# Performance work log

Hardware: AMD Instinct MI355X
Metric: run time of the kernel (lower is better)

Reference implementation:

```python
import jax, jax.numpy as jnp
import numpy as np

GROUP_SIZE = 16
OUT_FEATURES = 8192
IN_FEATURES = 8192


def block_dequantize_min_bit(x_quant_packed, normalization):
    """Unpack 3-bit values (8 values per 3 bytes) and dequantize per-group.

    x_quant_packed: [n_groups, group_size*3//8] int (byte values 0..255)
    normalization:  [n_groups, 1] float
    returns flat float32 vector of length n_groups*group_size.
    """
    normalization = normalization.astype(jnp.float32)
    packed_width = x_quant_packed.shape[1]
    group_size = packed_width * 8 // 3
    b = x_quant_packed.astype(jnp.int32).reshape(-1, 3)
    b0, b1, b2 = b[:, 0], b[:, 1], b[:, 2]
    v0 = (b0 >> 5) & 7
    v1 = (b0 >> 2) & 7
    v2 = ((b0 & 3) << 1) | ((b1 >> 7) & 1)
    v3 = (b1 >> 4) & 7
    v4 = (b1 >> 1) & 7
    v5 = ((b1 & 1) << 2) | ((b2 >> 6) & 3)
    v6 = (b2 >> 3) & 7
    v7 = b2 & 7
    unpacked = jnp.stack([v0, v1, v2, v3, v4, v5, v6, v7], axis=1)  # [-1, 8]
    x_quant = unpacked.reshape(-1, group_size).astype(jnp.float32)
    x_norm = x_quant / 7.0
    x = x_norm * 2.0 * normalization - normalization
    return x.reshape(-1)


def setup_inputs() -> dict:
    key = jax.random.key(0)
    k1, k2, k3, k4 = jax.random.split(key, 4)
    n_groups = OUT_FEATURES * IN_FEATURES // GROUP_SIZE
    x = jax.random.normal(k1, (64, IN_FEATURES), dtype=jnp.float32)
    weight_q3 = jax.random.randint(k2, (n_groups, GROUP_SIZE * 3 // 8), 0, 256, dtype=jnp.int32)
    # positive per-group max-abs scales (quantizer stores abs().max())
    weight_norm = jax.random.uniform(k3, (n_groups, 1), dtype=jnp.float32, minval=0.01, maxval=1.0)
    bias = jax.random.normal(k4, (OUT_FEATURES,), dtype=jnp.float32)
    return {"x": x, "weight_q3": weight_q3, "weight_norm": weight_norm, "bias": bias}


def reference(x, weight_q3, weight_norm, bias):
    w = block_dequantize_min_bit(weight_q3, weight_norm).reshape(OUT_FEATURES, IN_FEATURES)
    # F.linear: y = x @ W^T + b
    return jnp.einsum('bi,oi->bo', x, w) + bias
```

## Files before the change

kernel.cpp:

```cpp
#include <hip/hip_runtime.h>
#include <hip/hip_bf16.h>


#define BATCH   64
#define IN_F    8192
#define OUT_F   8192

#define PK_BYTES 6144
#define PA_BYTES 8192
#define BUF_BYTES (PK_BYTES + PA_BYTES)

typedef __attribute__((ext_vector_type(8))) short bf16x8;
typedef __attribute__((ext_vector_type(4))) float f32x4;

__device__ __forceinline__ ushort f2bf(float f) {
  union { float f; unsigned u; } a; a.f = f;
  unsigned r = a.u + 0x7fffu + ((a.u >> 16) & 1u);
  return (ushort)(r >> 16);
}

__device__ __forceinline__ void gl_lds16(const void* g, void* l) {
  __builtin_amdgcn_global_load_lds((const __attribute__((address_space(1))) void*)g,
                                   (__attribute__((address_space(3))) void*)l, 16, 0, 0);
}

__global__ void __launch_bounds__(256) xcvt_kernel(const float* __restrict__ x,
                                                   ushort* __restrict__ xb) {
  int i = blockIdx.x * 256 + threadIdx.x;
  float4 v = ((const float4*)x)[i];
  ushort4 o;
  o.x = f2bf(v.x); o.y = f2bf(v.y); o.z = f2bf(v.z); o.w = f2bf(v.w);
  ((ushort4*)xb)[i] = o;
}

__device__ __forceinline__ bf16x8 dqfrag(int b0, int b1, int b2, float nrm) {
  float c1 = nrm * (2.0f / 7.0f);
  float c0 = nrm;
  int v0 = (b0 >> 5) & 7;
  int v1 = (b0 >> 2) & 7;
  int v2 = ((b0 & 3) << 1) | ((b1 >> 7) & 1);
  int v3 = (b1 >> 4) & 7;
  int v4 = (b1 >> 1) & 7;
  int v5 = ((b1 & 1) << 2) | ((b2 >> 6) & 3);
  int v6 = (b2 >> 3) & 7;
  int v7 = b2 & 7;
  union { __hip_bfloat162 h[4]; bf16x8 v; } r;
  r.h[0] = __float22bfloat162_rn(make_float2(fmaf((float)v0, c1, -c0), fmaf((float)v1, c1, -c0)));
  r.h[1] = __float22bfloat162_rn(make_float2(fmaf((float)v2, c1, -c0), fmaf((float)v3, c1, -c0)));
  r.h[2] = __float22bfloat162_rn(make_float2(fmaf((float)v4, c1, -c0), fmaf((float)v5, c1, -c0)));
  r.h[3] = __float22bfloat162_rn(make_float2(fmaf((float)v6, c1, -c0), fmaf((float)v7, c1, -c0)));
  return r.v;
}

template <int KS>
__global__ void __launch_bounds__(256) gemm3b_kernel(const ushort* __restrict__ xb,
                                                     const int* __restrict__ wq,
                                                     const float* __restrict__ wnorm,
                                                     float* __restrict__ partial) {
  constexpr int K_SLICE = IN_F / KS;
  constexpr int NTILE   = K_SLICE / 64;
  constexpr int NGROW   = K_SLICE / 16;

  __shared__ __align__(16) char  LDS[2][BUF_BYTES];
  __shared__ __align__(16) float NRM[64 * NGROW];

  const int tid  = threadIdx.x;
  const int lane = tid & 63;
  const int w    = tid >> 6;
  const int l15  = lane & 15;
  const int h    = lane >> 4;
  const int nb64 = blockIdx.x * 64;
  const int s    = blockIdx.y;
  const int kbase = s * K_SLICE;
  const int kg0   = kbase >> 4;

  const char*  wqp = (const char*)wq + (size_t)nb64 * 12288 + (size_t)kg0 * 24;
  const float* wnp = wnorm + (size_t)nb64 * 512 + kg0;
  const char*  xbp = (const char*)xb + (size_t)kbase * 2;

  f32x4 acc[4];
  #pragma unroll
  for (int m = 0; m < 4; ++m) acc[m] = (f32x4){0.f, 0.f, 0.f, 0.f};

  {
    constexpr int ROWB = NGROW * 4;
    constexpr int NDM  = (64 * ROWB) / 4096;
    #pragma unroll
    for (int i = 0; i < NDM; ++i) {
      int t   = tid * 16 + i * 4096;
      int row = t / ROWB;
      int off = t % ROWB;
      float4 v = *(const float4*)((const char*)wnp + (size_t)row * 2048 + off);
      *(float4*)((char*)NRM + t) = v;
    }
  }

#define STAGE_PK_CHUNK(BUF, KT, C)                                            \
  do {                                                                        \
    int t   = (C) * 1024 + lane * 16;                                         \
    int row = (int)(((unsigned)t * 43691u) >> 22);                            \
    int off = t - row * 96;                                                   \
    gl_lds16(wqp + (size_t)row * 12288 + (KT) * 96 + off,                     \
             &LDS[BUF][(C) * 1024]);                                          \
  } while (0)

#define STAGE(BUF, KT)                                                        \
  do {                                                                        \
    STAGE_PK_CHUNK(BUF, KT, w);                                               \
    if (w < 2) STAGE_PK_CHUNK(BUF, KT, 4 + w);                                \
    _Pragma("unroll")                                                         \
    for (int i = 0; i < 2; ++i) {                                             \
      int row = (tid >> 3) + i * 32;                                          \
      int c   = tid & 7;                                                      \
      int cs  = c ^ (row & 7);                                                \
      gl_lds16(xbp + (size_t)row * (IN_F * 2) + (KT) * 128 + cs * 16,         \
               &LDS[BUF][PK_BYTES + i * 4096 + w * 1024]);                    \
    }                                                                         \
  } while (0)

#define COMPUTE(BUF, KT)                                                      \
  do {                                                                        \
    const char* pk = &LDS[BUF][0];                                            \
    const char* pa = &LDS[BUF][PK_BYTES];                                     \
    const int r_loc = w * 16 + l15;                                           \
    _Pragma("unroll")                                                         \
    for (int ks = 0; ks < 2; ++ks) {                                          \
      bf16x8 af[4];                                                           \
      _Pragma("unroll")                                                       \
      for (int m = 0; m < 4; ++m) {                                           \
        int row = m * 16 + l15;                                               \
        int cch = ks * 4 + h;                                                 \
        af[m] = *(const bf16x8*)(pa + row * 128 + ((cch ^ (row & 7)) * 16));  \
      }                                                                       \
      int g = ks * 2 + (h >> 1);                                              \
      const uint* p = (const uint*)(pk + r_loc * 96 + g * 24 + (h & 1) * 12); \
      bf16x8 bfr = dqfrag(p[0], p[1], p[2], NRM[r_loc * NGROW + (KT) * 4 + g]); \
      _Pragma("unroll")                                                       \
      for (int m = 0; m < 4; ++m)                                             \
        acc[m] = __builtin_amdgcn_mfma_f32_16x16x32_bf16(af[m], bfr, acc[m],  \
                                                         0, 0, 0);            \
    }                                                                         \
  } while (0)

  STAGE(0, 0);

  #pragma unroll
  for (int kt = 0; kt < NTILE; ++kt) {
    __syncthreads();
    if (kt + 1 < NTILE) STAGE((kt + 1) & 1, kt + 1);
    COMPUTE(kt & 1, kt);
  }

#undef STAGE
#undef STAGE_PK_CHUNK
#undef COMPUTE

  float* pout = partial + (size_t)s * BATCH * OUT_F;
  const int col = nb64 + w * 16 + l15;
  #pragma unroll
  for (int m = 0; m < 4; ++m) {
    int rowb = m * 16 + h * 4;
    #pragma unroll
    for (int r = 0; r < 4; ++r)
      pout[(size_t)(rowb + r) * OUT_F + col] = acc[m][r];
  }
}

template <int KS>
__global__ void __launch_bounds__(256) reduce_kernel(const float* __restrict__ partial,
                                                     const float* __restrict__ bias,
                                                     float* __restrict__ out) {
  int i = blockIdx.x * 256 + threadIdx.x;
  float4 a = ((const float4*)partial)[i];
  #pragma unroll
  for (int s2 = 1; s2 < KS; ++s2) {
    float4 b = ((const float4*)partial)[i + s2 * (BATCH * OUT_F / 4)];
    a.x += b.x; a.y += b.y; a.z += b.z; a.w += b.w;
  }
  float4 bv = ((const float4*)bias)[i & (OUT_F / 4 - 1)];
  a.x += bv.x; a.y += bv.y; a.z += bv.z; a.w += bv.w;
  ((float4*)out)[i] = a;
}

extern "C" void kernel_launch(void* const* d_in, const int* in_sizes, int n_in,
                              void* d_out, int out_size, void* d_ws, size_t ws_size,
                              hipStream_t stream) {
  const float* x     = (const float*)d_in[0];
  const int*   wq    = (const int*)d_in[1];
  const float* wnorm = (const float*)d_in[2];
  const float* bias  = (const float*)d_in[3];
  float* out = (float*)d_out;

  const size_t xb_bytes = (size_t)BATCH * IN_F * 2;
  ushort* xb      = (ushort*)d_ws;
  float*  partial = (float*)((char*)d_ws + xb_bytes);

  hipLaunchKernelGGL(xcvt_kernel, dim3(BATCH * IN_F / 4 / 256), dim3(256), 0, stream, x, xb);

  const size_t slice_bytes = (size_t)BATCH * OUT_F * 4;
  if (ws_size >= xb_bytes + 16 * slice_bytes) {
    hipLaunchKernelGGL((gemm3b_kernel<16>), dim3(OUT_F / 64, 16), dim3(256), 0, stream,
                       xb, wq, wnorm, partial);
    hipLaunchKernelGGL((reduce_kernel<16>), dim3(BATCH * OUT_F / 4 / 256), dim3(256), 0, stream,
                       partial, bias, out);
  } else if (ws_size >= xb_bytes + 8 * slice_bytes) {
    hipLaunchKernelGGL((gemm3b_kernel<8>), dim3(OUT_F / 64, 8), dim3(256), 0, stream,
                       xb, wq, wnorm, partial);
    hipLaunchKernelGGL((reduce_kernel<8>), dim3(BATCH * OUT_F / 4 / 256), dim3(256), 0, stream,
                       partial, bias, out);
  } else {
    hipLaunchKernelGGL((gemm3b_kernel<4>), dim3(OUT_F / 64, 4), dim3(256), 0, stream,
                       xb, wq, wnorm, partial);
    hipLaunchKernelGGL((reduce_kernel<4>), dim3(BATCH * OUT_F / 4 / 256), dim3(256), 0, stream,
                       partial, bias, out);
  }
}
```

Baseline: 47.26 us.

## Widen GEMM block tile to 128 output columns and transpose norm staging

Each block now covers 128 output features instead of 64, so every warp dequantizes two 16-column weight fragments and runs 8 MFMAs per k-step while reusing the same activation fragments. The aim is to halve redundant activation tile loads from LDS and global memory and raise MFMA density per block. The per-group norm cache is stored transposed (group-major), so reads during compute are contiguous across lanes. In exchange the grid has half as many blocks (1024 at KS=16), LDS per block roughly doubles and accumulator registers double, which can lower occupancy.

```diff
diff --git a/kernel.cpp b/kernel.cpp
--- a/kernel.cpp
+++ b/kernel.cpp
@@ -6,7 +6,7 @@
 #define IN_F    8192
 #define OUT_F   8192
 
-#define PK_BYTES 6144
+#define PK_BYTES 12288
 #define PA_BYTES 8192
 #define BUF_BYTES (PK_BYTES + PA_BYTES)
 
@@ -60,54 +60,55 @@
   constexpr int K_SLICE = IN_F / KS;
   constexpr int NTILE   = K_SLICE / 64;
   constexpr int NGROW   = K_SLICE / 16;
+  constexpr int QPR     = NGROW / 4;
 
   __shared__ __align__(16) char  LDS[2][BUF_BYTES];
-  __shared__ __align__(16) float NRM[64 * NGROW];
+  __shared__ __align__(16) float NRM[NGROW * 128];
 
   const int tid  = threadIdx.x;
   const int lane = tid & 63;
   const int w    = tid >> 6;
   const int l15  = lane & 15;
   const int h    = lane >> 4;
-  const int nb64 = blockIdx.x * 64;
+  const int nb128 = blockIdx.x * 128;
   const int s    = blockIdx.y;
   const int kbase = s * K_SLICE;
   const int kg0   = kbase >> 4;
 
-  const char*  wqp = (const char*)wq + (size_t)nb64 * 12288 + (size_t)kg0 * 24;
-  const float* wnp = wnorm + (size_t)nb64 * 512 + kg0;
-  const char*  xbp = (const char*)xb + (size_t)kbase * 2;
-
-  f32x4 acc[4];
-  #pragma unroll
-  for (int m = 0; m < 4; ++m) acc[m] = (f32x4){0.f, 0.f, 0.f, 0.f};
+  const char* wqp = (const char*)wq + (size_t)nb128 * 12288 + (size_t)kg0 * 24;
+  const char* xbp = (const char*)xb + (size_t)kbase * 2;
+
+  f32x4 acc[2][4];
+  #pragma unroll
+  for (int n = 0; n < 2; ++n)
+    #pragma unroll
+    for (int m = 0; m < 4; ++m) acc[n][m] = (f32x4){0.f, 0.f, 0.f, 0.f};
 
   {
-    constexpr int ROWB = NGROW * 4;
-    constexpr int NDM  = (64 * ROWB) / 4096;
+    const float4* wn4 = (const float4*)wnorm + (size_t)nb128 * 128 + (kg0 >> 2);
     #pragma unroll
-    for (int i = 0; i < NDM; ++i) {
-      int t   = tid * 16 + i * 4096;
-      int row = t / ROWB;
-      int off = t % ROWB;
-      float4 v = *(const float4*)((const char*)wnp + (size_t)row * 2048 + off);
-      *(float4*)((char*)NRM + t) = v;
+    for (int j = 0; j < QPR / 2; ++j) {
+      int f    = j * 256 + tid;
+      int row  = f / QPR;
+      int quad = f % QPR;
+      float4 v = wn4[(size_t)row * 128 + quad];
+      NRM[(quad * 4 + 0) * 128 + row] = v.x;
+      NRM[(quad * 4 + 1) * 128 + row] = v.y;
+      NRM[(quad * 4 + 2) * 128 + row] = v.z;
+      NRM[(quad * 4 + 3) * 128 + row] = v.w;
     }
   }
-
-#define STAGE_PK_CHUNK(BUF, KT, C)                                            \
-  do {                                                                        \
-    int t   = (C) * 1024 + lane * 16;                                         \
-    int row = (int)(((unsigned)t * 43691u) >> 22);                            \
-    int off = t - row * 96;                                                   \
-    gl_lds16(wqp + (size_t)row * 12288 + (KT) * 96 + off,                     \
-             &LDS[BUF][(C) * 1024]);                                          \
-  } while (0)
 
 #define STAGE(BUF, KT)                                                        \
   do {                                                                        \
-    STAGE_PK_CHUNK(BUF, KT, w);                                               \
-    if (w < 2) STAGE_PK_CHUNK(BUF, KT, 4 + w);                                \
+    _Pragma("unroll")                                                         \
+    for (int i = 0; i < 3; ++i) {                                             \
+      int t   = tid * 16 + i * 4096;                                          \
+      int row = (int)(((unsigned)t * 43691u) >> 22);                \
+      int off = t - row * 96;                                                 \
+      gl_lds16(wqp + (size_t)row * 12288 + (KT) * 96 + off,                   \
+               &LDS[BUF][i * 4096 + w * 1024]);                               \
+    }                                                                         \
     _Pragma("unroll")                                                         \
     for (int i = 0; i < 2; ++i) {                                             \
       int row = (tid >> 3) + i * 32;                                          \
@@ -122,7 +123,6 @@
   do {                                                                        \
     const char* pk = &LDS[BUF][0];                                            \
     const char* pa = &LDS[BUF][PK_BYTES];                                     \
-    const int r_loc = w * 16 + l15;                                           \
     _Pragma("unroll")                                                         \
     for (int ks = 0; ks < 2; ++ks) {                                          \
       bf16x8 af[4];                                                           \
@@ -132,13 +132,20 @@
         int cch = ks * 4 + h;                                                 \
         af[m] = *(const bf16x8*)(pa + row * 128 + ((cch ^ (row & 7)) * 16));  \
       }                                                                       \
-      int g = ks * 2 + (h >> 1);                                              \
-      const uint* p = (const uint*)(pk + r_loc * 96 + g * 24 + (h & 1) * 12); \
-      bf16x8 bfr = dqfrag(p[0], p[1], p[2], NRM[r_loc * NGROW + (KT) * 4 + g]); \
+      bf16x8 bfr[2];                                                          \
+      _Pragma("unroll")                                                       \
+      for (int n = 0; n < 2; ++n) {                                           \
+        int r_loc = w * 32 + n * 16 + l15;                                    \
+        int g = ks * 2 + (h >> 1);                                            \
+        const uint* p = (const uint*)(pk + r_loc * 96 + g * 24 + (h & 1) * 12); \
+        bfr[n] = dqfrag(p[0], p[1], p[2], NRM[((KT) * 4 + g) * 128 + r_loc]); \
+      }                                                                       \
       _Pragma("unroll")                                                       \
       for (int m = 0; m < 4; ++m)                                             \
-        acc[m] = __builtin_amdgcn_mfma_f32_16x16x32_bf16(af[m], bfr, acc[m],  \
-                                                         0, 0, 0);            \
+        _Pragma("unroll")                                                     \
+        for (int n = 0; n < 2; ++n)                                           \
+          acc[n][m] = __builtin_amdgcn_mfma_f32_16x16x32_bf16(af[m], bfr[n],  \
+                                                              acc[n][m], 0, 0, 0); \
     }                                                                         \
   } while (0)
 
@@ -152,17 +159,19 @@
   }
 
 #undef STAGE
-#undef STAGE_PK_CHUNK
 #undef COMPUTE
 
   float* pout = partial + (size_t)s * BATCH * OUT_F;
-  const int col = nb64 + w * 16 + l15;
-  #pragma unroll
-  for (int m = 0; m < 4; ++m) {
-    int rowb = m * 16 + h * 4;
+  #pragma unroll
+  for (int n = 0; n < 2; ++n) {
+    int col = nb128 + w * 32 + n * 16 + l15;
     #pragma unroll
-    for (int r = 0; r < 4; ++r)
-      pout[(size_t)(rowb + r) * OUT_F + col] = acc[m][r];
+    for (int m = 0; m < 4; ++m) {
+      int rowb = m * 16 + h * 4;
+      #pragma unroll
+      for (int r = 0; r < 4; ++r)
+        pout[(size_t)(rowb + r) * OUT_F + col] = acc[n][m][r];
+    }
   }
 }
 
@@ -199,17 +208,17 @@
 
   const size_t slice_bytes = (size_t)BATCH * OUT_F * 4;
   if (ws_size >= xb_bytes + 16 * slice_bytes) {
-    hipLaunchKernelGGL((gemm3b_kernel<16>), dim3(OUT_F / 64, 16), dim3(256), 0, stream,
+    hipLaunchKernelGGL((gemm3b_kernel<16>), dim3(OUT_F / 128, 16), dim3(256), 0, stream,
                        xb, wq, wnorm, partial);
     hipLaunchKernelGGL((reduce_kernel<16>), dim3(BATCH * OUT_F / 4 / 256), dim3(256), 0, stream,
                        partial, bias, out);
   } else if (ws_size >= xb_bytes + 8 * slice_bytes) {
-    hipLaunchKernelGGL((gemm3b_kernel<8>), dim3(OUT_F / 64, 8), dim3(256), 0, stream,
+    hipLaunchKernelGGL((gemm3b_kernel<8>), dim3(OUT_F / 128, 8), dim3(256), 0, stream,
                        xb, wq, wnorm, partial);
     hipLaunchKernelGGL((reduce_kernel<8>), dim3(BATCH * OUT_F / 4 / 256), dim3(256), 0, stream,
                        partial, bias, out);
   } else {
-    hipLaunchKernelGGL((gemm3b_kernel<4>), dim3(OUT_F / 64, 4), dim3(256), 0, stream,
+    hipLaunchKernelGGL((gemm3b_kernel<4>), dim3(OUT_F / 128, 4), dim3(256), 0, stream,
                        xb, wq, wnorm, partial);
     hipLaunchKernelGGL((reduce_kernel<4>), dim3(BATCH * OUT_F / 4 / 256), dim3(256), 0, stream,
                        partial, bias, out);
```

Result: no change. 47.60 us (+0.7%).
